# Optimization experiments

Hardware: AMD Instinct MI355X
Metric: run time of the kernel (lower is better)

## Reference

```python
import jax, jax.numpy as jnp
import numpy as np

DIM = 1024
HEADS = 16
DIM_HEAD = DIM // HEADS

def setup_inputs() -> dict:
    key = jax.random.key(0)
    k1, k2, k3 = jax.random.split(key, 3)
    x = jax.random.normal(k1, (2, 2048, DIM), dtype=jnp.float32)
    # nn.Linear(dim, 3*dim, bias=False): weight [3*dim, dim]; y = x @ W.T
    W_qkv = jax.random.normal(k2, (3 * DIM, DIM), dtype=jnp.float32) * (1.0 / np.sqrt(DIM))
    W_out = jax.random.normal(k3, (DIM, DIM), dtype=jnp.float32) * (1.0 / np.sqrt(DIM))
    return {"x": x, "W_qkv": W_qkv, "W_out": W_out}

def reference(x, W_qkv, W_out):
    b, s, _ = x.shape
    scale = DIM_HEAD ** -0.5
    qkv = x @ W_qkv.T                              # [b, s, 3*dim]
    q, k, v = jnp.split(qkv, 3, axis=-1)
    def to_heads(t):
        return t.reshape(b, s, HEADS, DIM_HEAD).transpose(0, 2, 1, 3)  # [b,h,s,d]
    q, k, v = map(to_heads, (q, k, v))
    scores = jnp.einsum('bhid,bhjd->bhij', q, k) * scale
    causal_mask = jnp.triu(jnp.ones((s, s), dtype=bool), k=1)
    scores = jnp.where(causal_mask, -jnp.inf, scores)
    attn = jax.nn.softmax(scores, axis=-1)
    out = jnp.einsum('bhij,bhjd->bhid', attn, v)
    out = out.transpose(0, 2, 1, 3).reshape(b, s, HEADS * DIM_HEAD)
    return out @ W_out.T
```

## Files before the change

kernel.cpp:

```cpp
#include <hip/hip_runtime.h>
#include <hip/hip_bf16.h>
#include <math.h>

using bf16 = __hip_bfloat16;
typedef __attribute__((ext_vector_type(8))) short bf16x8;
typedef __attribute__((ext_vector_type(4))) short bf16x4;
typedef __attribute__((ext_vector_type(4))) float f32x4;

static __device__ __forceinline__ void gl_lds16(const void* g, void* l) {
  __builtin_amdgcn_global_load_lds(
      (const __attribute__((address_space(1))) unsigned int*)g,
      (__attribute__((address_space(3))) unsigned int*)l, 16, 0, 0);
}

#define MFMA16 __builtin_amdgcn_mfma_f32_16x16x32_bf16
#define MFMA16K16 __builtin_amdgcn_mfma_f32_16x16x16bf16_1k

static __device__ __forceinline__ short f2bf(float f) {
  return (short)((__builtin_bit_cast(unsigned int, f) + 0x8000u) >> 16);
}

__global__ __launch_bounds__(256) void cvt_all(
    const float* __restrict__ x, const float* __restrict__ wqkv,
    const float* __restrict__ wout, bf16* __restrict__ xb,
    bf16* __restrict__ wqkvb, bf16* __restrict__ woutb) {
  const int blk = blockIdx.x;
  const float* src;
  bf16* dst;
  int base;
  if (blk < 4096) {
    src = x; dst = xb; base = blk;
  } else if (blk < 7168) {
    src = wqkv; dst = wqkvb; base = blk - 4096;
  } else {
    src = wout; dst = woutb; base = blk - 7168;
  }
  const int i = (base * 256 + threadIdx.x) * 4;
  const float4 v = *(const float4*)(src + i);
  bf16x4 o;
  o.x = f2bf(v.x);
  o.y = f2bf(v.y);
  o.z = f2bf(v.z);
  o.w = f2bf(v.w);
  *(bf16x4*)(dst + i) = o;
}

template <int K>
static __device__ __forceinline__ void gemm_bt_acc(
    const bf16* __restrict__ A, const bf16* __restrict__ B,
    int rowA0, int rowB0, bf16* As, bf16* Bs, f32x4 acc[4][4]) {
  const int t = threadIdx.x;
  const int w = t >> 6, l = t & 63;
  const int quad = l >> 4, l16 = l & 15;
  const int wm = (w >> 1) * 64, wn = (w & 1) * 64;
  const int c0 = t, c1 = t + 256;
  const bf16* a0 = A + (size_t)(rowA0 + (c0 >> 2)) * K + (c0 & 3) * 8;
  const bf16* a1 = A + (size_t)(rowA0 + (c1 >> 2)) * K + (c1 & 3) * 8;
  const bf16* b0 = B + (size_t)(rowB0 + (c0 >> 2)) * K + (c0 & 3) * 8;
  const bf16* b1 = B + (size_t)(rowB0 + (c1 >> 2)) * K + (c1 & 3) * 8;
  for (int k0 = 0; k0 < K; k0 += 32) {
    __syncthreads();
    gl_lds16(a0 + k0, As + c0 * 8);
    gl_lds16(a1 + k0, As + c1 * 8);
    gl_lds16(b0 + k0, Bs + c0 * 8);
    gl_lds16(b1 + k0, Bs + c1 * 8);
    __syncthreads();
    bf16x8 af[4], bg[4];
#pragma unroll
    for (int i = 0; i < 4; i++)
      af[i] = *(const bf16x8*)(As + (wm + i * 16 + l16) * 32 + quad * 8);
#pragma unroll
    for (int j = 0; j < 4; j++)
      bg[j] = *(const bf16x8*)(Bs + (wn + j * 16 + l16) * 32 + quad * 8);
#pragma unroll
    for (int i = 0; i < 4; i++)
#pragma unroll
      for (int j = 0; j < 4; j++)
        acc[i][j] = MFMA16(af[i], bg[j], acc[i][j], 0, 0, 0);
  }
}

__global__ __launch_bounds__(256) void qkv_gemm(
    const bf16* __restrict__ x, const bf16* __restrict__ Wqkv,
    bf16* __restrict__ Qb, bf16* __restrict__ Kb, bf16* __restrict__ Vt) {
  __shared__ bf16 As[128 * 32];
  __shared__ bf16 Bs[128 * 32];
  f32x4 acc[4][4];
#pragma unroll
  for (int i = 0; i < 4; i++)
#pragma unroll
    for (int j = 0; j < 4; j++) acc[i][j] = (f32x4){0.f, 0.f, 0.f, 0.f};
  const int bm = blockIdx.x, bn = blockIdx.y;
  gemm_bt_acc<1024>(x, Wqkv, bm * 128, bn * 128, As, Bs, acc);

  const int t = threadIdx.x, w = t >> 6, l = t & 63;
  const int quad = l >> 4, l16 = l & 15;
  const int wm = (w >> 1) * 64, wn = (w & 1) * 64;
#pragma unroll
  for (int i = 0; i < 4; i++) {
#pragma unroll
    for (int j = 0; j < 4; j++) {
      const int n = bn * 128 + wn + j * 16 + l16;
      const int which = n >> 10;
      const int nn = n & 1023;
      const int h = nn >> 6, d = nn & 63;
#pragma unroll
      for (int r = 0; r < 4; r++) {
        const int m = bm * 128 + wm + i * 16 + quad * 4 + r;
        const int b = m >> 11, s = m & 2047;
        const int bh = b * 16 + h;
        const bf16 v = __float2bfloat16(acc[i][j][r]);
        if (which == 0)
          Qb[((size_t)bh * 2048 + s) * 64 + d] = v;
        else if (which == 1)
          Kb[((size_t)bh * 2048 + s) * 64 + d] = v;
        else
          Vt[((size_t)bh * 64 + d) * 2048 + s] = v;
      }
    }
  }
}

__global__ __launch_bounds__(256) void attn_kernel(
    const bf16* __restrict__ Qb, const bf16* __restrict__ Kb,
    const bf16* __restrict__ Vt, bf16* __restrict__ attn) {
  __shared__ bf16 Qs[64 * 64];
  __shared__ bf16 Ks[128 * 64];
  __shared__ bf16 Vts[64 * 128];
  const int x = blockIdx.x;
  const int bh = x & 31;
  const int idx = x >> 5;
  const int qt = (idx < 16) ? idx : 47 - idx;
  const int q0 = qt * 64;
  const int t = threadIdx.x, w = t >> 6, l = t & 63;
  const int quad = l >> 4, l16 = l & 15;
  const float c_exp2 = 0.18033688011f;

  const bf16* Qg = Qb + ((size_t)bh * 2048 + q0) * 64;
#pragma unroll
  for (int c = t; c < 512; c += 256) {
    const int row = c >> 3, pos = c & 7;
    gl_lds16(Qg + (row * 8 + (pos ^ (row & 7))) * 8, Qs + c * 8);
  }

  f32x4 oacc[4];
  float lsum = 0.f;
#pragma unroll
  for (int md = 0; md < 4; md++) oacc[md] = (f32x4){0.f, 0.f, 0.f, 0.f};

  const int njj = (qt + 2) >> 1;
  for (int jj = 0; jj < njj; jj++) {
    const int j0 = jj * 128;
    __syncthreads();
    const bf16* Kg = Kb + ((size_t)bh * 2048 + j0) * 64;
#pragma unroll
    for (int c = t; c < 1024; c += 256) {
      const int row = c >> 3, pos = c & 7;
      gl_lds16(Kg + (row * 8 + (pos ^ (row & 7))) * 8, Ks + c * 8);
    }
    const bf16* Vg = Vt + (size_t)bh * 64 * 2048 + j0;
#pragma unroll
    for (int c = t; c < 1024; c += 256) {
      const int d = c >> 4, pos = c & 15;
      gl_lds16(Vg + (size_t)d * 2048 + ((pos ^ (d & 15)) * 8), Vts + c * 8);
    }
    __syncthreads();

    f32x4 sacc[8];
#pragma unroll
    for (int mt = 0; mt < 8; mt++) sacc[mt] = (f32x4){0.f, 0.f, 0.f, 0.f};
#pragma unroll
    for (int kk = 0; kk < 2; kk++) {
      const int qrow = w * 16 + l16;
      const int qpos = (kk * 4 + quad) ^ (qrow & 7);
      bf16x8 qf = *(const bf16x8*)(Qs + qrow * 64 + qpos * 8);
#pragma unroll
      for (int mt = 0; mt < 8; mt++) {
        const int row = mt * 16 + l16;
        const int pos = (kk * 4 + quad) ^ (row & 7);
        bf16x8 kf = *(const bf16x8*)(Ks + row * 64 + pos * 8);
        sacc[mt] = MFMA16(kf, qf, sacc[mt], 0, 0, 0);
      }
    }

    bf16x4 pfrag[8];
    if (jj == njj - 1) {
      const int qi = q0 + w * 16 + l16;
#pragma unroll
      for (int mt = 0; mt < 8; mt++) {
        bf16x4 p4;
#pragma unroll
        for (int r = 0; r < 4; r++) {
          const int sg = j0 + mt * 16 + quad * 4 + r;
          float p = (sg <= qi) ? exp2f(sacc[mt][r] * c_exp2) : 0.f;
          lsum += p;
          p4[r] = f2bf(p);
        }
        pfrag[mt] = p4;
      }
    } else {
#pragma unroll
      for (int mt = 0; mt < 8; mt++) {
        bf16x4 p4;
#pragma unroll
        for (int r = 0; r < 4; r++) {
          const float p = exp2f(sacc[mt][r] * c_exp2);
          lsum += p;
          p4[r] = f2bf(p);
        }
        pfrag[mt] = p4;
      }
    }

#pragma unroll
    for (int kt = 0; kt < 8; kt++) {
#pragma unroll
      for (int md = 0; md < 4; md++) {
        const int d = md * 16 + l16;
        const int pos = (kt * 2 + (quad >> 1)) ^ (d & 15);
        bf16x4 va = *(const bf16x4*)(Vts + d * 128 + pos * 8 + (quad & 1) * 4);
        oacc[md] = MFMA16K16(va, pfrag[kt], oacc[md], 0, 0, 0);
      }
    }
  }

  lsum += __shfl_xor(lsum, 16, 64);
  lsum += __shfl_xor(lsum, 32, 64);
  const float inv = 1.0f / lsum;
  const int b = bh >> 4, h = bh & 15;
  const int srow = q0 + w * 16 + l16;
#pragma unroll
  for (int md = 0; md < 4; md++) {
    bf16x4 o4;
#pragma unroll
    for (int r = 0; r < 4; r++) o4[r] = f2bf(oacc[md][r] * inv);
    *(bf16x4*)(attn + ((size_t)b * 2048 + srow) * 1024 + h * 64 + md * 16 +
               quad * 4) = o4;
  }
}

__global__ __launch_bounds__(256) void out_gemm(
    const bf16* __restrict__ attn, const bf16* __restrict__ Wout,
    float* __restrict__ out) {
  __shared__ bf16 As[128 * 32];
  __shared__ bf16 Bs[128 * 32];
  f32x4 acc[4][4];
#pragma unroll
  for (int i = 0; i < 4; i++)
#pragma unroll
    for (int j = 0; j < 4; j++) acc[i][j] = (f32x4){0.f, 0.f, 0.f, 0.f};
  const int bm = blockIdx.x, bn = blockIdx.y;
  gemm_bt_acc<1024>(attn, Wout, bm * 128, bn * 128, As, Bs, acc);

  const int t = threadIdx.x, w = t >> 6, l = t & 63;
  const int quad = l >> 4, l16 = l & 15;
  const int wm = (w >> 1) * 64, wn = (w & 1) * 64;
#pragma unroll
  for (int i = 0; i < 4; i++) {
#pragma unroll
    for (int j = 0; j < 4; j++) {
      const int n = bn * 128 + wn + j * 16 + l16;
#pragma unroll
      for (int r = 0; r < 4; r++) {
        const int m = bm * 128 + wm + i * 16 + quad * 4 + r;
        out[(size_t)m * 1024 + n] = acc[i][j][r];
      }
    }
  }
}

extern "C" void kernel_launch(void* const* d_in, const int* in_sizes, int n_in,
                              void* d_out, int out_size, void* d_ws, size_t ws_size,
                              hipStream_t stream) {
  const float* x = (const float*)d_in[0];
  const float* Wqkv = (const float*)d_in[1];
  const float* Wout = (const float*)d_in[2];
  float* out = (float*)d_out;

  char* ws = (char*)d_ws;
  const size_t MB = 1024 * 1024;
  bf16* xb = (bf16*)(ws + 0 * MB);
  bf16* at = (bf16*)(ws + 0 * MB);
  bf16* Wqkvb = (bf16*)(ws + 8 * MB);
  bf16* Woutb = (bf16*)(ws + 14 * MB);
  bf16* Qb = (bf16*)(ws + 16 * MB);
  bf16* Kb = (bf16*)(ws + 24 * MB);
  bf16* Vt = (bf16*)(ws + 32 * MB);

  cvt_all<<<8192, 256, 0, stream>>>(x, Wqkv, Wout, xb, Wqkvb, Woutb);
  qkv_gemm<<<dim3(32, 24), 256, 0, stream>>>(xb, Wqkvb, Qb, Kb, Vt);
  attn_kernel<<<1024, 256, 0, stream>>>(Qb, Kb, Vt, at);
  out_gemm<<<dim3(32, 8), 256, 0, stream>>>(at, Woutb, out);
}
```

Baseline: 182.5 us.

## Fold softmax scale into Q, compute row sums via MFMA, retile output GEMM

Q is now multiplied by 0.125 when the QKV GEMM writes it, so attention can use __expf directly instead of a scaled exp2. The per-thread row sum and its cross-lane shuffles are replaced by an extra MFMA against a vector of bf16 ones. The bf16 pack is done with perm instructions. The output GEMM moves from 128x128 to 128x64 tiles with an inline loop, doubling the grid to fill more CUs at the cost of more redundant A loads. As before, the softmax does no max subtraction and relies on the input scale.

```diff
diff --git a/kernel.cpp b/kernel.cpp
--- a/kernel.cpp
+++ b/kernel.cpp
@@ -6,6 +6,7 @@
 typedef __attribute__((ext_vector_type(8))) short bf16x8;
 typedef __attribute__((ext_vector_type(4))) short bf16x4;
 typedef __attribute__((ext_vector_type(4))) float f32x4;
+typedef __attribute__((ext_vector_type(2))) int i32x2;
 
 static __device__ __forceinline__ void gl_lds16(const void* g, void* l) {
   __builtin_amdgcn_global_load_lds(
@@ -104,12 +105,13 @@
       const int which = n >> 10;
       const int nn = n & 1023;
       const int h = nn >> 6, d = nn & 63;
+      const float sc = (which == 0) ? 0.125f : 1.0f;
 #pragma unroll
       for (int r = 0; r < 4; r++) {
         const int m = bm * 128 + wm + i * 16 + quad * 4 + r;
         const int b = m >> 11, s = m & 2047;
         const int bh = b * 16 + h;
-        const bf16 v = __float2bfloat16(acc[i][j][r]);
+        const bf16 v = __float2bfloat16(acc[i][j][r] * sc);
         if (which == 0)
           Qb[((size_t)bh * 2048 + s) * 64 + d] = v;
         else if (which == 1)
@@ -134,7 +136,7 @@
   const int q0 = qt * 64;
   const int t = threadIdx.x, w = t >> 6, l = t & 63;
   const int quad = l >> 4, l16 = l & 15;
-  const float c_exp2 = 0.18033688011f;
+  const bf16x4 ones = {16256, 16256, 16256, 16256};
 
   const bf16* Qg = Qb + ((size_t)bh * 2048 + q0) * 64;
 #pragma unroll
@@ -144,7 +146,7 @@
   }
 
   f32x4 oacc[4];
-  float lsum = 0.f;
+  f32x4 lacc = (f32x4){0.f, 0.f, 0.f, 0.f};
 #pragma unroll
   for (int md = 0; md < 4; md++) oacc[md] = (f32x4){0.f, 0.f, 0.f, 0.f};
 
@@ -188,32 +190,37 @@
       const int qi = q0 + w * 16 + l16;
 #pragma unroll
       for (int mt = 0; mt < 8; mt++) {
-        bf16x4 p4;
+        unsigned rb[4];
 #pragma unroll
         for (int r = 0; r < 4; r++) {
           const int sg = j0 + mt * 16 + quad * 4 + r;
-          float p = (sg <= qi) ? exp2f(sacc[mt][r] * c_exp2) : 0.f;
-          lsum += p;
-          p4[r] = f2bf(p);
+          const float p = (sg <= qi) ? __expf(sacc[mt][r]) : 0.f;
+          rb[r] = __builtin_bit_cast(unsigned, p) + 0x8000u;
         }
-        pfrag[mt] = p4;
+        i32x2 pk;
+        pk.x = (int)__builtin_amdgcn_perm(rb[1], rb[0], 0x07060302u);
+        pk.y = (int)__builtin_amdgcn_perm(rb[3], rb[2], 0x07060302u);
+        pfrag[mt] = __builtin_bit_cast(bf16x4, pk);
       }
     } else {
 #pragma unroll
       for (int mt = 0; mt < 8; mt++) {
-        bf16x4 p4;
+        unsigned rb[4];
 #pragma unroll
         for (int r = 0; r < 4; r++) {
-          const float p = exp2f(sacc[mt][r] * c_exp2);
-          lsum += p;
-          p4[r] = f2bf(p);
+          const float p = __expf(sacc[mt][r]);
+          rb[r] = __builtin_bit_cast(unsigned, p) + 0x8000u;
         }
-        pfrag[mt] = p4;
+        i32x2 pk;
+        pk.x = (int)__builtin_amdgcn_perm(rb[1], rb[0], 0x07060302u);
+        pk.y = (int)__builtin_amdgcn_perm(rb[3], rb[2], 0x07060302u);
+        pfrag[mt] = __builtin_bit_cast(bf16x4, pk);
       }
     }
 
 #pragma unroll
     for (int kt = 0; kt < 8; kt++) {
+      lacc = MFMA16K16(ones, pfrag[kt], lacc, 0, 0, 0);
 #pragma unroll
       for (int md = 0; md < 4; md++) {
         const int d = md * 16 + l16;
@@ -224,9 +231,7 @@
     }
   }
 
-  lsum += __shfl_xor(lsum, 16, 64);
-  lsum += __shfl_xor(lsum, 32, 64);
-  const float inv = 1.0f / lsum;
+  const float inv = 1.0f / lacc[0];
   const int b = bh >> 4, h = bh & 15;
   const int srow = q0 + w * 16 + l16;
 #pragma unroll
@@ -243,23 +248,44 @@
     const bf16* __restrict__ attn, const bf16* __restrict__ Wout,
     float* __restrict__ out) {
   __shared__ bf16 As[128 * 32];
-  __shared__ bf16 Bs[128 * 32];
-  f32x4 acc[4][4];
+  __shared__ bf16 Bs[64 * 32];
+  f32x4 acc[4][2];
 #pragma unroll
   for (int i = 0; i < 4; i++)
 #pragma unroll
-    for (int j = 0; j < 4; j++) acc[i][j] = (f32x4){0.f, 0.f, 0.f, 0.f};
+    for (int j = 0; j < 2; j++) acc[i][j] = (f32x4){0.f, 0.f, 0.f, 0.f};
   const int bm = blockIdx.x, bn = blockIdx.y;
-  gemm_bt_acc<1024>(attn, Wout, bm * 128, bn * 128, As, Bs, acc);
-
   const int t = threadIdx.x, w = t >> 6, l = t & 63;
   const int quad = l >> 4, l16 = l & 15;
-  const int wm = (w >> 1) * 64, wn = (w & 1) * 64;
+  const int wm = (w >> 1) * 64, wn = (w & 1) * 32;
+  const int c0 = t, c1 = t + 256;
+  const bf16* a0 = attn + (size_t)(bm * 128 + (c0 >> 2)) * 1024 + (c0 & 3) * 8;
+  const bf16* a1 = attn + (size_t)(bm * 128 + (c1 >> 2)) * 1024 + (c1 & 3) * 8;
+  const bf16* b0 = Wout + (size_t)(bn * 64 + (t >> 2)) * 1024 + (t & 3) * 8;
+  for (int k0 = 0; k0 < 1024; k0 += 32) {
+    __syncthreads();
+    gl_lds16(a0 + k0, As + c0 * 8);
+    gl_lds16(a1 + k0, As + c1 * 8);
+    gl_lds16(b0 + k0, Bs + t * 8);
+    __syncthreads();
+    bf16x8 af[4], bg[2];
+#pragma unroll
+    for (int i = 0; i < 4; i++)
+      af[i] = *(const bf16x8*)(As + (wm + i * 16 + l16) * 32 + quad * 8);
+#pragma unroll
+    for (int j = 0; j < 2; j++)
+      bg[j] = *(const bf16x8*)(Bs + (wn + j * 16 + l16) * 32 + quad * 8);
+#pragma unroll
+    for (int i = 0; i < 4; i++)
+#pragma unroll
+      for (int j = 0; j < 2; j++)
+        acc[i][j] = MFMA16(af[i], bg[j], acc[i][j], 0, 0, 0);
+  }
 #pragma unroll
   for (int i = 0; i < 4; i++) {
 #pragma unroll
-    for (int j = 0; j < 4; j++) {
-      const int n = bn * 128 + wn + j * 16 + l16;
+    for (int j = 0; j < 2; j++) {
+      const int n = bn * 64 + wn + j * 16 + l16;
 #pragma unroll
       for (int r = 0; r < 4; r++) {
         const int m = bm * 128 + wm + i * 16 + quad * 4 + r;
@@ -290,5 +316,5 @@
   cvt_all<<<8192, 256, 0, stream>>>(x, Wqkv, Wout, xb, Wqkvb, Woutb);
   qkv_gemm<<<dim3(32, 24), 256, 0, stream>>>(xb, Wqkvb, Qb, Kb, Vt);
   attn_kernel<<<1024, 256, 0, stream>>>(Qb, Kb, Vt, at);
-  out_gemm<<<dim3(32, 8), 256, 0, stream>>>(at, Woutb, out);
-}
+  out_gemm<<<dim3(32, 16), 256, 0, stream>>>(at, Woutb, out);
+}
```

New measurement: 169.6 us. 1.08x faster.
